# Optimization experiments

Hardware: AMD Instinct MI355X
Metric: run time of the kernel (lower is better)

The kernel has to match this reference:

```python
import jax, jax.numpy as jnp
import numpy as np

HIDDEN = 768
HEADS = 12
HEAD_DIM = HIDDEN // HEADS


def setup_inputs() -> dict:
    key = jax.random.key(0)
    ks = jax.random.split(key, 9)
    B, S = 2, 2048
    scale = 1.0 / np.sqrt(HIDDEN)
    return {
        "hidden_states": jax.random.normal(ks[0], (B, S, HIDDEN), jnp.float32),
        "context": jax.random.normal(ks[1], (B, S, HIDDEN), jnp.float32),
        "attention_mask": jnp.zeros((B, 1, 1, S), jnp.float32),
        "Wq": jax.random.normal(ks[2], (HIDDEN, HIDDEN), jnp.float32) * scale,
        "bq": jnp.zeros((HIDDEN,), jnp.float32),
        "Wk": jax.random.normal(ks[3], (HIDDEN, HIDDEN), jnp.float32) * scale,
        "bk": jnp.zeros((HIDDEN,), jnp.float32),
        "Wv": jax.random.normal(ks[4], (HIDDEN, HIDDEN), jnp.float32) * scale,
        "bv": jnp.zeros((HIDDEN,), jnp.float32),
    }


def _split_heads(x):
    # [B, S, H*D] -> [B, H, S, D]
    B, S, _ = x.shape
    return x.reshape(B, S, HEADS, HEAD_DIM).transpose(0, 2, 1, 3)


def reference(hidden_states, context, attention_mask, Wq, bq, Wk, bk, Wv, bv):
    # torch Linear: y = x @ W^T + b
    q = _split_heads(hidden_states @ Wq.T + bq)   # [B,H,Sq,D]
    k = _split_heads(context @ Wk.T + bk)         # [B,H,Sk,D]
    v = _split_heads(context @ Wv.T + bv)         # [B,H,Sk,D]

    scores = jnp.einsum("bhqd,bhkd->bhqk", q, k)
    scores = scores / np.sqrt(HEAD_DIM + 1e-05)
    scores = scores + attention_mask
    probs = jax.nn.softmax(scores, axis=-1)       # dropout p=0 -> identity (eval)
    ctx = jnp.einsum("bhqk,bhkd->bhqd", probs, v) # [B,H,Sq,D]
    B, H, Sq, D = ctx.shape
    return ctx.transpose(0, 2, 1, 3).reshape(B, Sq, H * D)
```

## Files before the change

kernel.cpp:

```cpp
#include <hip/hip_runtime.h>
#include <hip/hip_bf16.h>
#include <math.h>

typedef short s16x8 __attribute__((ext_vector_type(8)));
typedef float f32x4 __attribute__((ext_vector_type(4)));
typedef _Float16 f16x4 __attribute__((ext_vector_type(4)));
typedef __fp16 fp16x2 __attribute__((ext_vector_type(2)));
typedef unsigned short u16;

#define NHEADS 12
#define SEQ 2048
#define NBH 24
#define KDIM 768
#define LOG2E 1.44269504088896f

#define SWZ(row, col) (((row) * 64) + ((col) ^ (((row) & 7) << 3)))

#define GLOAD_LDS16(g, l) __builtin_amdgcn_global_load_lds( \
    (const __attribute__((address_space(1))) unsigned int*)(g), \
    (__attribute__((address_space(3))) unsigned int*)(l), 16, 0, 0)

static __device__ __forceinline__ u16 f2bf(float f) {
    union { float f; unsigned u; } v; v.f = f;
    unsigned r = v.u + 0x7fffu + ((v.u >> 16) & 1u);
    return (u16)(r >> 16);
}
static __device__ __forceinline__ u16 f2h(float f) {
    union { _Float16 h; u16 u; } v; v.h = (_Float16)f;
    return v.u;
}
static __device__ __forceinline__ f16x4 pack4(float a, float b, float c, float d) {
    union { fp16x2 h2[2]; f16x4 h4; } u;
    u.h2[0] = __builtin_amdgcn_cvt_pkrtz(a, b);
    u.h2[1] = __builtin_amdgcn_cvt_pkrtz(c, d);
    return u.h4;
}

__global__ void cvt6_kernel(const float* __restrict__ s0, const float* __restrict__ s1,
                            const float* __restrict__ s2, const float* __restrict__ s3,
                            const float* __restrict__ s4, const float* __restrict__ s5,
                            u16* __restrict__ d0, u16* __restrict__ d1, u16* __restrict__ d2,
                            u16* __restrict__ d3, u16* __restrict__ d4, float* __restrict__ d5,
                            int n4a, int n4w, float qscl) {
    const int z = blockIdx.z;
    int i = blockIdx.x * blockDim.x + threadIdx.x;
    if (z == 5) {
        if (i < (2 * SEQ) / 4) {
            float4 f = ((const float4*)s5)[i];
            f.x *= LOG2E; f.y *= LOG2E; f.z *= LOG2E; f.w *= LOG2E;
            ((float4*)d5)[i] = f;
        }
        return;
    }
    const float* src = (z == 0) ? s0 : (z == 1) ? s1 : (z == 2) ? s2 : (z == 3) ? s3 : s4;
    u16* dst         = (z == 0) ? d0 : (z == 1) ? d1 : (z == 2) ? d2 : (z == 3) ? d3 : d4;
    const int n4     = (z < 2) ? n4a : n4w;
    const float scl  = (z == 2) ? qscl : 1.0f;
    if (i < n4) {
        float4 f = ((const float4*)src)[i];
        ushort4 o;
        o.x = f2bf(f.x * scl); o.y = f2bf(f.y * scl); o.z = f2bf(f.z * scl); o.w = f2bf(f.w * scl);
        ((ushort4*)dst)[i] = o;
    }
}

__launch_bounds__(256)
__global__ void qkv_gemm(const u16* __restrict__ X, const u16* __restrict__ C,
                         const u16* __restrict__ W0, const u16* __restrict__ W1, const u16* __restrict__ W2,
                         const float* __restrict__ b0, const float* __restrict__ b1, const float* __restrict__ b2,
                         u16* __restrict__ Qo, u16* __restrict__ Ko, u16* __restrict__ Vo, float qscl) {
    const int z = blockIdx.z;
    const u16* A    = (z == 0) ? X  : C;
    const u16* W    = (z == 0) ? W0 : (z == 1) ? W1 : W2;
    const float* bi = (z == 0) ? b0 : (z == 1) ? b1 : b2;
    u16* out        = (z == 0) ? Qo : (z == 1) ? Ko : Vo;
    const float bscl = (z == 0) ? qscl : 1.0f;

    __shared__ u16 As[2][128 * 64];
    __shared__ u16 Bs[2][128 * 64];

    const int tid  = threadIdx.x;
    const int lane = tid & 63;
    const int wid  = tid >> 6;
    const int wr = wid >> 1, wc = wid & 1;
    const int l15 = lane & 15, lh = lane >> 4;
    const int mBase = blockIdx.x * 128;
    const int nBase = blockIdx.y * 128;

    size_t aSrc[4], bSrc[4]; int ldsOffG[4];
    #pragma unroll
    for (int i = 0; i < 4; ++i) {
        int L = wid * 512 + i * 2048 + lane * 8;
        int row = L >> 6;
        int col = (L & 63) ^ ((row & 7) << 3);
        aSrc[i] = (size_t)(mBase + row) * KDIM + col;
        bSrc[i] = (size_t)(nBase + row) * KDIM + col;
        ldsOffG[i] = wid * 512 + i * 2048;
    }

    f32x4 acc[4][4] = {};

    #pragma unroll
    for (int i = 0; i < 4; ++i) {
        GLOAD_LDS16(&A[aSrc[i]], &As[0][ldsOffG[i]]);
        GLOAD_LDS16(&W[bSrc[i]], &Bs[0][ldsOffG[i]]);
    }

    const int NIT = KDIM / 64;
    for (int it = 0; it < NIT; ++it) {
        const int cur = it & 1;
        __syncthreads();
        if (it + 1 < NIT) {
            const int kb = (it + 1) * 64;
            #pragma unroll
            for (int i = 0; i < 4; ++i) {
                GLOAD_LDS16(&A[aSrc[i] + kb], &As[cur ^ 1][ldsOffG[i]]);
                GLOAD_LDS16(&W[bSrc[i] + kb], &Bs[cur ^ 1][ldsOffG[i]]);
            }
        }
        #pragma unroll
        for (int kk = 0; kk < 2; ++kk) {
            s16x8 af[4], bf[4];
            #pragma unroll
            for (int m = 0; m < 4; ++m)
                af[m] = *(const s16x8*)(&As[cur][SWZ(wr * 64 + m * 16 + l15, kk * 32 + lh * 8)]);
            #pragma unroll
            for (int n = 0; n < 4; ++n)
                bf[n] = *(const s16x8*)(&Bs[cur][SWZ(wc * 64 + n * 16 + l15, kk * 32 + lh * 8)]);
            #pragma unroll
            for (int m = 0; m < 4; ++m)
                #pragma unroll
                for (int n = 0; n < 4; ++n)
                    acc[m][n] = __builtin_amdgcn_mfma_f32_16x16x32_bf16(af[m], bf[n], acc[m][n], 0, 0, 0);
        }
    }

    if (z < 2) {
        #pragma unroll
        for (int m = 0; m < 4; ++m) {
            #pragma unroll
            for (int n = 0; n < 4; ++n) {
                int colg = nBase + wc * 64 + n * 16 + l15;
                float bv = bi[colg] * bscl;
                int h = colg >> 6, d = colg & 63;
                #pragma unroll
                for (int j = 0; j < 4; ++j) {
                    int rowg = mBase + wr * 64 + m * 16 + lh * 4 + j;
                    int b = rowg >> 11, s = rowg & 2047;
                    out[(((size_t)(b * NHEADS + h) * SEQ + s) << 6) + d] = f2bf(acc[m][n][j] + bv);
                }
            }
        }
    } else {
        #pragma unroll
        for (int m = 0; m < 4; ++m) {
            #pragma unroll
            for (int n = 0; n < 4; ++n) {
                int colg = nBase + wc * 64 + n * 16 + l15;
                float bv = bi[colg];
                int h = colg >> 6, d = colg & 63;
                int rowg0 = mBase + wr * 64 + m * 16 + lh * 4;
                int b = rowg0 >> 11, s = rowg0 & 2047;
                int sp = (s & ~0x3C) | (((s >> 2) & 3) << 4) | (((s >> 4) & 3) << 2);
                ushort4 o;
                o.x = f2h(acc[m][n][0] + bv);
                o.y = f2h(acc[m][n][1] + bv);
                o.z = f2h(acc[m][n][2] + bv);
                o.w = f2h(acc[m][n][3] + bv);
                *(ushort4*)(&out[(((size_t)(b * NHEADS + h) * 64 + d) << 11) + sp]) = o;
            }
        }
    }
}

template<bool SPLIT>
__launch_bounds__(512)
__global__ void attn_kernel(const u16* __restrict__ Qg, const u16* __restrict__ Kg,
                            const u16* __restrict__ Vg,
                            const float* __restrict__ maskL, float* __restrict__ out,
                            float* __restrict__ Opart, float* __restrict__ MLpart) {
    __shared__ u16 Ks[2][64 * 64];
    __shared__ u16 Vt[2][64 * 64];

    const int tid  = threadIdx.x;
    const int lane = tid & 63;
    const int wid  = tid >> 6;
    const int bh = blockIdx.y;
    const int b = bh / NHEADS;
    const int h = bh % NHEADS;
    const int q0 = blockIdx.x * 128 + wid * 16;
    const int l15 = lane & 15, lh = lane >> 4;
    const int z = SPLIT ? blockIdx.z : 0;
    const int NT = SPLIT ? (SEQ / 128) : (SEQ / 64);
    const int tile0 = z * NT;

    const int srow = tid >> 3;
    const int scol = ((tid & 7) * 8) ^ ((srow & 7) << 3);
    const size_t kSrc = (((size_t)bh * SEQ + srow) << 6) + scol + ((size_t)tile0 << 12);
    const size_t vSrc = (((size_t)bh * 64 + srow) << 11) + scol + (size_t)tile0 * 64;
    const int ldsBase = wid * 512;

    s16x8 qf[2];
    #pragma unroll
    for (int kk = 0; kk < 2; ++kk)
        qf[kk] = *(const s16x8*)(&Qg[(((size_t)bh * SEQ + q0 + l15) << 6) + kk * 32 + lh * 8]);

    f32x4 oacc[4] = {};
    float mrun = -1e30f, lrun = 0.f;

    GLOAD_LDS16(&Kg[kSrc], &Ks[0][ldsBase]);
    GLOAD_LDS16(&Vg[vSrc], &Vt[0][ldsBase]);

    for (int t = 0; t < NT; ++t) {
        const int cur = t & 1;
        __syncthreads();
        if (t + 1 < NT) {
            GLOAD_LDS16(&Kg[kSrc + ((size_t)(t + 1) << 12)], &Ks[cur ^ 1][ldsBase]);
            GLOAD_LDS16(&Vg[vSrc + (size_t)(t + 1) * 64],    &Vt[cur ^ 1][ldsBase]);
        }

        f32x4 sacc[4] = {};
        __builtin_amdgcn_s_setprio(1);
        #pragma unroll
        for (int kk = 0; kk < 2; ++kk) {
            #pragma unroll
            for (int n = 0; n < 4; ++n) {
                s16x8 kf = *(const s16x8*)(&Ks[cur][SWZ(n * 16 + l15, kk * 32 + lh * 8)]);
                sacc[n] = __builtin_amdgcn_mfma_f32_16x16x32_bf16(kf, qf[kk], sacc[n], 0, 0, 0);
            }
        }
        __builtin_amdgcn_s_setprio(0);
        #pragma unroll
        for (int n = 0; n < 4; ++n) {
            float4 mv = *(const float4*)(&maskL[(size_t)b * SEQ + (tile0 + t) * 64 + n * 16 + lh * 4]);
            sacc[n][0] += mv.x; sacc[n][1] += mv.y; sacc[n][2] += mv.z; sacc[n][3] += mv.w;
        }

        float tmax = sacc[0][0];
        #pragma unroll
        for (int n = 0; n < 4; ++n)
            #pragma unroll
            for (int j = 0; j < 4; ++j)
                tmax = fmaxf(tmax, sacc[n][j]);
        tmax = fmaxf(tmax, __shfl_xor(tmax, 16));
        tmax = fmaxf(tmax, __shfl_xor(tmax, 32));

        if (!__all(tmax - mrun <= 11.0f)) {
            float mnew = fmaxf(mrun, tmax);
            float alpha = __builtin_amdgcn_exp2f(mrun - mnew);
            lrun *= alpha;
            #pragma unroll
            for (int nd = 0; nd < 4; ++nd)
                #pragma unroll
                for (int j = 0; j < 4; ++j)
                    oacc[nd][j] *= alpha;
            mrun = mnew;
        }

        float rs = 0.f;
        f16x4 pf[4];
        #pragma unroll
        for (int n = 0; n < 4; ++n) {
            float p0 = __builtin_amdgcn_exp2f(sacc[n][0] - mrun);
            float p1 = __builtin_amdgcn_exp2f(sacc[n][1] - mrun);
            float p2 = __builtin_amdgcn_exp2f(sacc[n][2] - mrun);
            float p3 = __builtin_amdgcn_exp2f(sacc[n][3] - mrun);
            rs += (p0 + p1) + (p2 + p3);
            pf[n] = pack4(p0, p1, p2, p3);
        }
        rs += __shfl_xor(rs, 16);
        rs += __shfl_xor(rs, 32);
        lrun += rs;

        __builtin_amdgcn_s_setprio(1);
        #pragma unroll
        for (int kk = 0; kk < 2; ++kk) {
            #pragma unroll
            for (int nd = 0; nd < 4; ++nd) {
                s16x8 v2 = *(const s16x8*)(&Vt[cur][SWZ(nd * 16 + l15, lh * 16 + kk * 8)]);
                union { s16x8 s8; f16x4 h4[2]; } u; u.s8 = v2;
                oacc[nd] = __builtin_amdgcn_mfma_f32_16x16x16f16(u.h4[0], pf[2 * kk],     oacc[nd], 0, 0, 0);
                oacc[nd] = __builtin_amdgcn_mfma_f32_16x16x16f16(u.h4[1], pf[2 * kk + 1], oacc[nd], 0, 0, 0);
            }
        }
        __builtin_amdgcn_s_setprio(0);
    }

    const float inv = 1.0f / lrun;
    const int s = q0 + l15;
    if (!SPLIT) {
        #pragma unroll
        for (int nd = 0; nd < 4; ++nd) {
            float4 o;
            o.x = oacc[nd][0] * inv; o.y = oacc[nd][1] * inv;
            o.z = oacc[nd][2] * inv; o.w = oacc[nd][3] * inv;
            *(float4*)(&out[(size_t)(b * SEQ + s) * (NHEADS * 64) + h * 64 + nd * 16 + lh * 4]) = o;
        }
    } else {
        const size_t rbase = ((size_t)(z * NBH + bh) * SEQ + s);
        #pragma unroll
        for (int nd = 0; nd < 4; ++nd) {
            float4 o;
            o.x = oacc[nd][0] * inv; o.y = oacc[nd][1] * inv;
            o.z = oacc[nd][2] * inv; o.w = oacc[nd][3] * inv;
            *(float4*)(&Opart[rbase * 64 + nd * 16 + lh * 4]) = o;
        }
        if (lh == 0)
            *(float2*)(&MLpart[rbase * 2]) = make_float2(mrun, lrun);
    }
}

__global__ void combine_kernel(const float* __restrict__ Opart, const float* __restrict__ MLpart,
                               float* __restrict__ out) {
    int gid = blockIdx.x * 256 + threadIdx.x;
    int row = gid >> 4, d4 = gid & 15;
    float2 ml0 = ((const float2*)MLpart)[row];
    float2 ml1 = ((const float2*)MLpart)[NBH * SEQ + row];
    float m = fmaxf(ml0.x, ml1.x);
    float w0 = __builtin_amdgcn_exp2f(ml0.x - m) * ml0.y;
    float w1 = __builtin_amdgcn_exp2f(ml1.x - m) * ml1.y;
    float inv = 1.0f / (w0 + w1);
    w0 *= inv; w1 *= inv;
    float4 o0 = *(const float4*)(&Opart[(size_t)row * 64 + d4 * 4]);
    float4 o1 = *(const float4*)(&Opart[(size_t)NBH * SEQ * 64 + (size_t)row * 64 + d4 * 4]);
    float4 o;
    o.x = o0.x * w0 + o1.x * w1; o.y = o0.y * w0 + o1.y * w1;
    o.z = o0.z * w0 + o1.z * w1; o.w = o0.w * w0 + o1.w * w1;
    int bh = row >> 11, s = row & 2047;
    int b = bh / NHEADS, hh = bh % NHEADS;
    *(float4*)(&out[(size_t)(b * SEQ + s) * (NHEADS * 64) + hh * 64 + d4 * 4]) = o;
}

extern "C" void kernel_launch(void* const* d_in, const int* in_sizes, int n_in,
                              void* d_out, int out_size, void* d_ws, size_t ws_size,
                              hipStream_t stream) {
    const float* hidden  = (const float*)d_in[0];
    const float* context = (const float*)d_in[1];
    const float* mask    = (const float*)d_in[2];
    const float* Wq = (const float*)d_in[3];
    const float* bq = (const float*)d_in[4];
    const float* Wk = (const float*)d_in[5];
    const float* bk = (const float*)d_in[6];
    const float* Wv = (const float*)d_in[7];
    const float* bv = (const float*)d_in[8];
    float* out = (float*)d_out;

    char* ws = (char*)d_ws;
    const size_t XSZ = (size_t)4096 * 768 * 2;
    const size_t WSZ = (size_t)768 * 768 * 2;
    u16* X16  = (u16*)(ws);
    u16* C16  = (u16*)(ws + XSZ);
    u16* W16q = (u16*)(ws + 2 * XSZ);
    u16* W16k = (u16*)(ws + 2 * XSZ + WSZ);
    u16* W16v = (u16*)(ws + 2 * XSZ + 2 * WSZ);
    u16* Q16  = (u16*)(ws + 2 * XSZ + 3 * WSZ);
    u16* K16  = (u16*)(ws + 3 * XSZ + 3 * WSZ);
    u16* V16  = (u16*)(ws + 4 * XSZ + 3 * WSZ);
    const size_t MASKL_OFF = 5 * XSZ + 3 * WSZ;
    float* maskL = (float*)(ws + MASKL_OFF);
    const size_t OPART_OFF = MASKL_OFF + 2 * SEQ * sizeof(float) + 256;
    float* Opart = (float*)(ws + OPART_OFF);
    const size_t ML_OFF = OPART_OFF + (size_t)2 * NBH * SEQ * 64 * 4;
    float* MLpart = (float*)(ws + ML_OFF);
    const size_t WS_NEED_SPLIT = ML_OFF + (size_t)2 * NBH * SEQ * 2 * 4;

    const float qscl = (float)((1.0 / sqrt(64.0 + 1e-5)) * 1.44269504088896);

    const int n4x = 4096 * 768 / 4;
    const int n4w = 768 * 768 / 4;
    cvt6_kernel<<<dim3((n4x + 255) / 256, 1, 6), 256, 0, stream>>>(
        hidden, context, Wq, Wk, Wv, mask,
        X16, C16, W16q, W16k, W16v, maskL, n4x, n4w, qscl);

    qkv_gemm<<<dim3(4096 / 128, 768 / 128, 3), 256, 0, stream>>>(
        X16, C16, W16q, W16k, W16v, bq, bk, bv, Q16, K16, V16, qscl);

    if (ws_size >= WS_NEED_SPLIT) {
        attn_kernel<true><<<dim3(SEQ / 128, NBH, 2), 512, 0, stream>>>(
            Q16, K16, V16, maskL, out, Opart, MLpart);
        combine_kernel<<<(NBH * SEQ * 16) / 256, 256, 0, stream>>>(Opart, MLpart, out);
    } else {
        attn_kernel<false><<<dim3(SEQ / 128, NBH, 1), 512, 0, stream>>>(
            Q16, K16, V16, maskL, out, Opart, MLpart);
    }
}
```

Measured before the change: 98.79 us.

## Transpose Q/K projection MFMA for vector stores; stage mask in LDS; defer row reductions

For the Q/K projections the MFMA operands are swapped so each lane holds four consecutive head-dim outputs, which allows packed ushort4 stores and a float4 bias load in place of scalar scattered stores. The attention kernel copies its slice of the mask into LDS once and uses it to initialise the score accumulators, removing a per-tile global load and the separate add. The row-max cross-lane shuffles now run only on the rescale path, and the row-sum shuffles are moved out of the loop to run once at the end. The extra 8KB of LDS may lower occupancy, and the rescale test now uses each lane's partial max, which stays correct but changes when rescaling happens.

```diff
diff --git a/kernel.cpp b/kernel.cpp
--- a/kernel.cpp
+++ b/kernel.cpp
@@ -120,35 +120,45 @@
         }
         #pragma unroll
         for (int kk = 0; kk < 2; ++kk) {
-            s16x8 af[4], bf[4];
+            s16x8 xf[4], wf[4];
             #pragma unroll
             for (int m = 0; m < 4; ++m)
-                af[m] = *(const s16x8*)(&As[cur][SWZ(wr * 64 + m * 16 + l15, kk * 32 + lh * 8)]);
+                xf[m] = *(const s16x8*)(&As[cur][SWZ(wr * 64 + m * 16 + l15, kk * 32 + lh * 8)]);
             #pragma unroll
             for (int n = 0; n < 4; ++n)
-                bf[n] = *(const s16x8*)(&Bs[cur][SWZ(wc * 64 + n * 16 + l15, kk * 32 + lh * 8)]);
-            #pragma unroll
-            for (int m = 0; m < 4; ++m)
+                wf[n] = *(const s16x8*)(&Bs[cur][SWZ(wc * 64 + n * 16 + l15, kk * 32 + lh * 8)]);
+            if (z < 2) {
                 #pragma unroll
-                for (int n = 0; n < 4; ++n)
-                    acc[m][n] = __builtin_amdgcn_mfma_f32_16x16x32_bf16(af[m], bf[n], acc[m][n], 0, 0, 0);
+                for (int m = 0; m < 4; ++m)
+                    #pragma unroll
+                    for (int n = 0; n < 4; ++n)
+                        acc[m][n] = __builtin_amdgcn_mfma_f32_16x16x32_bf16(wf[n], xf[m], acc[m][n], 0, 0, 0);
+            } else {
+                #pragma unroll
+                for (int m = 0; m < 4; ++m)
+                    #pragma unroll
+                    for (int n = 0; n < 4; ++n)
+                        acc[m][n] = __builtin_amdgcn_mfma_f32_16x16x32_bf16(xf[m], wf[n], acc[m][n], 0, 0, 0);
+            }
         }
     }
 
     if (z < 2) {
         #pragma unroll
         for (int m = 0; m < 4; ++m) {
+            int sg = mBase + wr * 64 + m * 16 + l15;
+            int b = sg >> 11, s = sg & 2047;
             #pragma unroll
             for (int n = 0; n < 4; ++n) {
-                int colg = nBase + wc * 64 + n * 16 + l15;
-                float bv = bi[colg] * bscl;
-                int h = colg >> 6, d = colg & 63;
-                #pragma unroll
-                for (int j = 0; j < 4; ++j) {
-                    int rowg = mBase + wr * 64 + m * 16 + lh * 4 + j;
-                    int b = rowg >> 11, s = rowg & 2047;
-                    out[(((size_t)(b * NHEADS + h) * SEQ + s) << 6) + d] = f2bf(acc[m][n][j] + bv);
-                }
+                int d0 = nBase + wc * 64 + n * 16 + lh * 4;
+                int h = d0 >> 6, d = d0 & 63;
+                float4 bv = *(const float4*)(&bi[d0]);
+                ushort4 o;
+                o.x = f2bf(acc[m][n][0] + bv.x * bscl);
+                o.y = f2bf(acc[m][n][1] + bv.y * bscl);
+                o.z = f2bf(acc[m][n][2] + bv.z * bscl);
+                o.w = f2bf(acc[m][n][3] + bv.w * bscl);
+                *(ushort4*)(&out[(((size_t)(b * NHEADS + h) * SEQ + s) << 6) + d]) = o;
             }
         }
     } else {
@@ -181,6 +191,7 @@
                             float* __restrict__ Opart, float* __restrict__ MLpart) {
     __shared__ u16 Ks[2][64 * 64];
     __shared__ u16 Vt[2][64 * 64];
+    __shared__ float maskLds[2048];
 
     const int tid  = threadIdx.x;
     const int lane = tid & 63;
@@ -194,6 +205,9 @@
     const int NT = SPLIT ? (SEQ / 128) : (SEQ / 64);
     const int tile0 = z * NT;
 
+    for (int i = tid * 4; i < NT * 64; i += 512 * 4)
+        *(float4*)(&maskLds[i]) = *(const float4*)(&maskL[(size_t)b * SEQ + (tile0 << 6) + i]);
+
     const int srow = tid >> 3;
     const int scol = ((tid & 7) * 8) ^ ((srow & 7) << 3);
     const size_t kSrc = (((size_t)bh * SEQ + srow) << 6) + scol + ((size_t)tile0 << 12);
@@ -219,7 +233,12 @@
             GLOAD_LDS16(&Vg[vSrc + (size_t)(t + 1) * 64],    &Vt[cur ^ 1][ldsBase]);
         }
 
-        f32x4 sacc[4] = {};
+        f32x4 sacc[4];
+        #pragma unroll
+        for (int n = 0; n < 4; ++n) {
+            float4 mv = *(const float4*)(&maskLds[t * 64 + n * 16 + lh * 4]);
+            sacc[n][0] = mv.x; sacc[n][1] = mv.y; sacc[n][2] = mv.z; sacc[n][3] = mv.w;
+        }
         __builtin_amdgcn_s_setprio(1);
         #pragma unroll
         for (int kk = 0; kk < 2; ++kk) {
@@ -230,11 +249,6 @@
             }
         }
         __builtin_amdgcn_s_setprio(0);
-        #pragma unroll
-        for (int n = 0; n < 4; ++n) {
-            float4 mv = *(const float4*)(&maskL[(size_t)b * SEQ + (tile0 + t) * 64 + n * 16 + lh * 4]);
-            sacc[n][0] += mv.x; sacc[n][1] += mv.y; sacc[n][2] += mv.z; sacc[n][3] += mv.w;
-        }
 
         float tmax = sacc[0][0];
         #pragma unroll
@@ -242,11 +256,11 @@
             #pragma unroll
             for (int j = 0; j < 4; ++j)
                 tmax = fmaxf(tmax, sacc[n][j]);
-        tmax = fmaxf(tmax, __shfl_xor(tmax, 16));
-        tmax = fmaxf(tmax, __shfl_xor(tmax, 32));
 
         if (!__all(tmax - mrun <= 11.0f)) {
-            float mnew = fmaxf(mrun, tmax);
+            float rmax = fmaxf(tmax, __shfl_xor(tmax, 16));
+            rmax = fmaxf(rmax, __shfl_xor(rmax, 32));
+            float mnew = fmaxf(mrun, rmax);
             float alpha = __builtin_amdgcn_exp2f(mrun - mnew);
             lrun *= alpha;
             #pragma unroll
@@ -257,7 +271,6 @@
             mrun = mnew;
         }
 
-        float rs = 0.f;
         f16x4 pf[4];
         #pragma unroll
         for (int n = 0; n < 4; ++n) {
@@ -265,12 +278,9 @@
             float p1 = __builtin_amdgcn_exp2f(sacc[n][1] - mrun);
             float p2 = __builtin_amdgcn_exp2f(sacc[n][2] - mrun);
             float p3 = __builtin_amdgcn_exp2f(sacc[n][3] - mrun);
-            rs += (p0 + p1) + (p2 + p3);
+            lrun += (p0 + p1) + (p2 + p3);
             pf[n] = pack4(p0, p1, p2, p3);
         }
-        rs += __shfl_xor(rs, 16);
-        rs += __shfl_xor(rs, 32);
-        lrun += rs;
 
         __builtin_amdgcn_s_setprio(1);
         #pragma unroll
@@ -285,6 +295,9 @@
         }
         __builtin_amdgcn_s_setprio(0);
     }
+
+    lrun += __shfl_xor(lrun, 16);
+    lrun += __shfl_xor(lrun, 32);
 
     const float inv = 1.0f / lrun;
     const int s = q0 + l15;
```

Measured after the change: 93.03 us. 1.06x faster.
